# Optimization experiments

Hardware: AMD Instinct MI355X
Metric: run time of the kernel (lower is better)

## Reference

```python
import jax, jax.numpy as jnp
import numpy as np

N_HEAD = 8
D_IN = 128
D_KEY = 32
B = 65536
EPS = 1e-5
TEMP = float(D_KEY ** 0.5)


def _xavier(k, shape):
    fan_out, fan_in = shape
    limit = float(np.sqrt(6.0 / (fan_in + fan_out)))
    return jax.random.uniform(k, shape, jnp.float32, -limit, limit)


def setup_inputs() -> dict:
    key = jax.random.key(0)
    ks = jax.random.split(key, 6)
    return {
        "h_emb": jax.random.normal(ks[0], (B, D_IN), jnp.float32),
        "r_emb": jax.random.normal(ks[1], (B, D_IN), jnp.float32),
        "w_h": _xavier(ks[2], (N_HEAD * D_IN, D_IN)),
        "w_r": _xavier(ks[3], (N_HEAD * D_IN, D_IN)),
        "k_h": _xavier(ks[4], (D_KEY, D_IN)),
        "k_r": _xavier(ks[5], (D_KEY, D_IN)),
        "ln_gamma": jnp.ones((D_IN,), jnp.float32),
        "ln_beta": jnp.zeros((D_IN,), jnp.float32),
        "mode": 0,  # 0 == 'normal'
    }


def reference(h_emb, r_emb, w_h, w_r, k_h, k_r, ln_gamma, ln_beta, mode):
    # mode == 0 <=> 'normal': h_batch = h_emb.shape[0], r_batch = r_emb.shape[0]
    residual = h_emb                                     # [B, D]
    hb = h_emb.shape[0]
    rb = r_emb.shape[0]
    # linear projections to n_head copies: [1, B, H, D]
    h1 = (h_emb @ w_h.T).reshape(-1, hb, N_HEAD, D_IN)
    r1 = (r_emb @ w_r.T).reshape(-1, rb, N_HEAD, D_IN)
    # small key projections: [1, B, H, K]
    h1k = h1 @ k_h.T
    r1k = r1 @ k_r.T
    # tiny HxH attention per batch element: [1, B, H, H]
    xattn = jnp.einsum('gbhk,gbjk->gbhj', h1k / TEMP, r1k)
    g, b = xattn.shape[0], xattn.shape[1]
    xattn = jax.nn.softmax(xattn.reshape(g, b, N_HEAD * N_HEAD), axis=-1)
    xattn = xattn.reshape(g, b, N_HEAD, N_HEAD)
    h_x = xattn.sum(axis=-1)[..., None]                  # [1, B, H, 1]
    r_x = xattn.sum(axis=-2)[..., None]                  # [1, B, H, 1]
    # weighted combine + head-sum + residual: [1, B, D]
    t = (h1 * h_x + r1 * r_x).sum(axis=-2) + residual
    # LayerNorm (applied because norm_flag is False in the original)
    mu = t.mean(axis=-1, keepdims=True)
    var = ((t - mu) ** 2).mean(axis=-1, keepdims=True)
    return ln_gamma * (t - mu) / jnp.sqrt(var + EPS) + ln_beta
```

## Files before the change

kernel.cpp:

```cpp
#include <hip/hip_runtime.h>
#include <hip/hip_fp16.h>

#define TEMP_INV 0.17677669529663687f

typedef _Float16 f16x8 __attribute__((ext_vector_type(8)));
typedef float    f32x4 __attribute__((ext_vector_type(4)));

__device__ __forceinline__ ushort f2h(float x){
  __half h = __float2half(x);
  return __half_as_ushort(h);
}
__device__ __forceinline__ ushort4 f4h(float4 v){
  ushort4 o; o.x=f2h(v.x); o.y=f2h(v.y); o.z=f2h(v.z); o.w=f2h(v.w); return o;
}
__device__ __forceinline__ f16x8 cvt8(float4 a, float4 b){
  f16x8 r;
  r[0]=(_Float16)a.x; r[1]=(_Float16)a.y; r[2]=(_Float16)a.z; r[3]=(_Float16)a.w;
  r[4]=(_Float16)b.x; r[5]=(_Float16)b.y; r[6]=(_Float16)b.z; r[7]=(_Float16)b.w;
  return r;
}
__device__ __forceinline__ f16x8 vscale(f16x8 v, _Float16 s){
  f16x8 r;
  #pragma unroll
  for (int i=0;i<8;i++) r[i] = v[i]*s;
  return r;
}

__global__ void conv_w_kernel(const float* __restrict__ wh,
                              const float* __restrict__ wr,
                              ushort* __restrict__ w16h,
                              ushort* __restrict__ w16r){
  int t = blockIdx.x * 256 + threadIdx.x;
  int R  = t >> 5;
  int c4 = t & 31;
  int h  = R >> 7, np = R & 127;
  int kq = c4 >> 1, pos = (c4 & 1) * 4;
  int dst = ((h*16 + kq)*128 + np)*8 + pos;
  float4 a = ((const float4*)wh)[t];
  *(ushort4*)&w16h[dst] = f4h(a);
  float4 b = ((const float4*)wr)[t];
  *(ushort4*)&w16r[dst] = f4h(b);
}

__global__ void make_cw_kernel(const float* __restrict__ wh, const float* __restrict__ wr,
                               const float* __restrict__ kh, const float* __restrict__ kr,
                               ushort* __restrict__ cwh, ushort* __restrict__ cwr){
  int m  = blockIdx.x >> 5;
  int h  = (blockIdx.x >> 2) & 7;
  int iq = blockIdx.x & 3;
  const float* w = m ? wr : wh;
  const float* k = m ? kr : kh;
  ushort* cw = m ? cwr : cwh;

  extern __shared__ char smem[];
  float* w_s = (float*)smem;
  float* k_s = w_s + 128*32;
  int t = threadIdx.x;

  #pragma unroll
  for (int p=0;p<4;p++){
    int f = t + p*256;
    int d = f >> 3, c4 = f & 7;
    *(float4*)&w_s[d*32 + c4*4] =
        *(const float4*)&w[(size_t)(h*128 + d)*128 + iq*32 + c4*4];
  }
  #pragma unroll
  for (int p=0;p<4;p++){
    int f = t + p*256;
    ((float4*)k_s)[f] = ((const float4*)k)[f];
  }
  __syncthreads();

  int il  = t & 31;
  int kk0 = t >> 5;
  float acc[4] = {0.f,0.f,0.f,0.f};
  for (int d=0; d<128; d++){
    float wv = w_s[d*32 + il];
    #pragma unroll
    for (int j=0;j<4;j++) acc[j] += k_s[(kk0 + 8*j)*128 + d] * wv;
  }
  int i = iq*32 + il;
  #pragma unroll
  for (int j=0;j<4;j++){
    int n = h*32 + kk0 + 8*j;
    cw[(size_t)((i>>3)*256 + n)*8 + (i&7)] = f2h(acc[j]);
  }
}

__global__ __launch_bounds__(256,2) void xattn_fused(
    const float* __restrict__ h_emb, const float* __restrict__ r_emb,
    const ushort* __restrict__ w16h, const ushort* __restrict__ w16r,
    const ushort* __restrict__ cwh,  const ushort* __restrict__ cwr,
    const float* __restrict__ gamma, const float* __restrict__ beta,
    float* __restrict__ out)
{
  extern __shared__ char smem[];
  float* hk  = (float*)smem;
  float* rk  = hk + 32*292;
  float* hxs = rk + 32*292;
  float* rxs = hxs + 288;
  float* red = rxs + 288;

  const int t  = threadIdx.x;
  const int b0 = blockIdx.x * 32;
  const int l  = t & 63, w = t >> 6;
  const int g  = l >> 4, c = l & 15;

  f16x8 ah[2][4], ar[2][4];
  #pragma unroll
  for (int mt=0; mt<2; mt++){
    const float* ph = h_emb + ((size_t)(b0 + mt*16 + c))*128 + g*8;
    const float* pr = r_emb + ((size_t)(b0 + mt*16 + c))*128 + g*8;
    #pragma unroll
    for (int ks=0; ks<4; ks++){
      float4 lo  = *(const float4*)(ph + ks*32);
      float4 hi  = *(const float4*)(ph + ks*32 + 4);
      ah[mt][ks] = cvt8(lo, hi);
      float4 lo2 = *(const float4*)(pr + ks*32);
      float4 hi2 = *(const float4*)(pr + ks*32 + 4);
      ar[mt][ks] = cvt8(lo2, hi2);
    }
  }

  f32x4 aH[2][4] = {};
  f32x4 aR[2][4] = {};
  {
    const ushort* pH = cwh + ((size_t)g*256 + w*64 + c)*8;
    const ushort* pR = cwr + ((size_t)g*256 + w*64 + c)*8;
    #pragma unroll
    for (int ks=0; ks<4; ks++){
      #pragma unroll
      for (int nt=0; nt<4; nt++){
        f16x8 bh = *(const f16x8*)(pH + ((size_t)ks*1024 + nt*16)*8);
        f16x8 br = *(const f16x8*)(pR + ((size_t)ks*1024 + nt*16)*8);
        aH[0][nt] = __builtin_amdgcn_mfma_f32_16x16x32_f16(ah[0][ks], bh, aH[0][nt],0,0,0);
        aH[1][nt] = __builtin_amdgcn_mfma_f32_16x16x32_f16(ah[1][ks], bh, aH[1][nt],0,0,0);
        aR[0][nt] = __builtin_amdgcn_mfma_f32_16x16x32_f16(ar[0][ks], br, aR[0][nt],0,0,0);
        aR[1][nt] = __builtin_amdgcn_mfma_f32_16x16x32_f16(ar[1][ks], br, aR[1][nt],0,0,0);
      }
    }
  }

  #pragma unroll
  for (int mt=0; mt<2; mt++)
    #pragma unroll
    for (int nt=0; nt<4; nt++){
      int n  = w*64 + nt*16 + c;
      int hh = n >> 5, kk = n & 31;
      #pragma unroll
      for (int reg=0; reg<4; reg++){
        int e = mt*16 + g*4 + reg;
        hk[e*292 + hh*36 + kk] = aH[mt][nt][reg];
        rk[e*292 + hh*36 + kk] = aR[mt][nt][reg];
      }
    }
  __syncthreads();

  {
    int e = t >> 3, hr = t & 7;
    const float* hkr = &hk[e*292 + hr*36];
    float4 hv4[8];
    #pragma unroll
    for (int q=0;q<8;q++) hv4[q] = *(const float4*)&hkr[q*4];

    float lg[8];
    #pragma unroll
    for (int j=0;j<8;j++){
      const float* rkr = &rk[e*292 + j*36];
      float s = 0.f;
      #pragma unroll
      for (int q=0;q<8;q++){
        float4 rv = *(const float4*)&rkr[q*4];
        s += hv4[q].x*rv.x + hv4[q].y*rv.y + hv4[q].z*rv.z + hv4[q].w*rv.w;
      }
      lg[j] = s * TEMP_INV;
    }
    float mx = lg[0];
    #pragma unroll
    for (int j=1;j<8;j++) mx = fmaxf(mx, lg[j]);
    mx = fmaxf(mx, __shfl_xor(mx, 1));
    mx = fmaxf(mx, __shfl_xor(mx, 2));
    mx = fmaxf(mx, __shfl_xor(mx, 4));
    float p[8]; float srow = 0.f;
    #pragma unroll
    for (int j=0;j<8;j++){ p[j] = __expf(lg[j]-mx); srow += p[j]; }
    float S = srow;
    S += __shfl_xor(S, 1); S += __shfl_xor(S, 2); S += __shfl_xor(S, 4);
    float inv = 1.0f / S;
    hxs[e*9 + hr] = srow * inv;

    #pragma unroll
    for (int j=0;j<8;j++){
      p[j] += __shfl_xor(p[j], 1);
      p[j] += __shfl_xor(p[j], 2);
      p[j] += __shfl_xor(p[j], 4);
    }
    float cs = p[0];
    #pragma unroll
    for (int j=1;j<8;j++) cs = (hr==j) ? p[j] : cs;
    rxs[e*9 + hr] = cs * inv;
  }
  __syncthreads();

  const int col0 = w*32;
  f32x4 tacc[2][2] = {};
  {
    const ushort* bH = w16h + ((size_t)g*128 + col0 + c)*8;
    const ushort* bR = w16r + ((size_t)g*128 + col0 + c)*8;
    #pragma unroll
    for (int h=0; h<8; h++){
      _Float16 h0 = (_Float16)hxs[c*9 + h];
      _Float16 h1 = (_Float16)hxs[(16+c)*9 + h];
      _Float16 r0 = (_Float16)rxs[c*9 + h];
      _Float16 r1 = (_Float16)rxs[(16+c)*9 + h];
      #pragma unroll
      for (int ks=0; ks<4; ks++){
        size_t off = (size_t)(h*16 + ks*4)*128*8;
        f16x8 a0 = vscale(ah[0][ks], h0);
        f16x8 a1 = vscale(ah[1][ks], h1);
        f16x8 b0v = *(const f16x8*)(bH + off);
        f16x8 b1v = *(const f16x8*)(bH + off + 16*8);
        tacc[0][0] = __builtin_amdgcn_mfma_f32_16x16x32_f16(a0, b0v, tacc[0][0],0,0,0);
        tacc[1][0] = __builtin_amdgcn_mfma_f32_16x16x32_f16(a1, b0v, tacc[1][0],0,0,0);
        tacc[0][1] = __builtin_amdgcn_mfma_f32_16x16x32_f16(a0, b1v, tacc[0][1],0,0,0);
        tacc[1][1] = __builtin_amdgcn_mfma_f32_16x16x32_f16(a1, b1v, tacc[1][1],0,0,0);
        f16x8 c0 = vscale(ar[0][ks], r0);
        f16x8 c1 = vscale(ar[1][ks], r1);
        f16x8 d0v = *(const f16x8*)(bR + off);
        f16x8 d1v = *(const f16x8*)(bR + off + 16*8);
        tacc[0][0] = __builtin_amdgcn_mfma_f32_16x16x32_f16(c0, d0v, tacc[0][0],0,0,0);
        tacc[1][0] = __builtin_amdgcn_mfma_f32_16x16x32_f16(c1, d0v, tacc[1][0],0,0,0);
        tacc[0][1] = __builtin_amdgcn_mfma_f32_16x16x32_f16(c0, d1v, tacc[0][1],0,0,0);
        tacc[1][1] = __builtin_amdgcn_mfma_f32_16x16x32_f16(c1, d1v, tacc[1][1],0,0,0);
      }
    }
  }

  #pragma unroll
  for (int mt=0; mt<2; mt++)
    #pragma unroll
    for (int reg=0; reg<4; reg++){
      int row = mt*16 + g*4 + reg;
      const float* resid = h_emb + ((size_t)(b0+row))*128 + col0 + c;
      tacc[mt][0][reg] += resid[0];
      tacc[mt][1][reg] += resid[16];
    }

  #pragma unroll
  for (int mt=0; mt<2; mt++)
    #pragma unroll
    for (int reg=0; reg<4; reg++){
      float v0 = tacc[mt][0][reg], v1 = tacc[mt][1][reg];
      float a = v0 + v1, b2 = v0*v0 + v1*v1;
      #pragma unroll
      for (int m=1; m<16; m<<=1){
        a  += __shfl_xor(a,  m);
        b2 += __shfl_xor(b2, m);
      }
      if (c == 0){
        int row = mt*16 + g*4 + reg;
        red[row*8 + w*2]     = a;
        red[row*8 + w*2 + 1] = b2;
      }
    }
  __syncthreads();

  float gam0 = gamma[col0 + c],      bet0 = beta[col0 + c];
  float gam1 = gamma[col0 + 16 + c], bet1 = beta[col0 + 16 + c];
  #pragma unroll
  for (int mt=0; mt<2; mt++)
    #pragma unroll
    for (int reg=0; reg<4; reg++){
      int row = mt*16 + g*4 + reg;
      float S1 = red[row*8+0] + red[row*8+2] + red[row*8+4] + red[row*8+6];
      float S2 = red[row*8+1] + red[row*8+3] + red[row*8+5] + red[row*8+7];
      float mu  = S1 * 0.0078125f;
      float var = S2 * 0.0078125f - mu*mu;
      float rs  = rsqrtf(var + 1e-5f);
      float* po = out + ((size_t)(b0+row))*128 + col0 + c;
      po[0]  = gam0*((tacc[mt][0][reg]-mu)*rs) + bet0;
      po[16] = gam1*((tacc[mt][1][reg]-mu)*rs) + bet1;
    }
}

extern "C" void kernel_launch(void* const* d_in, const int* in_sizes, int n_in,
                              void* d_out, int out_size, void* d_ws, size_t ws_size,
                              hipStream_t stream){
  const float* h_emb = (const float*)d_in[0];
  const float* r_emb = (const float*)d_in[1];
  const float* w_h   = (const float*)d_in[2];
  const float* w_r   = (const float*)d_in[3];
  const float* k_h   = (const float*)d_in[4];
  const float* k_r   = (const float*)d_in[5];
  const float* gamma = (const float*)d_in[6];
  const float* beta  = (const float*)d_in[7];
  float* out = (float*)d_out;

  ushort* w16h = (ushort*)d_ws;
  ushort* w16r = w16h + 131072;
  ushort* cwh  = w16r + 131072;
  ushort* cwr  = cwh + 32768;

  conv_w_kernel<<<128, 256, 0, stream>>>(w_h, w_r, w16h, w16r);
  make_cw_kernel<<<64, 256, 32768, stream>>>(w_h, w_r, k_h, k_r, cwh, cwr);
  xattn_fused<<<2048, 256, 78080, stream>>>(h_emb, r_emb, w16h, w16r,
                                            cwh, cwr, gamma, beta, out);
}
```

Baseline: 209.6 us.

## Split fused kernel into attention and projection kernels with larger row tiles

Merges the two weight-prep kernels into one launch. Splits the fused kernel into an attention kernel (16 rows per block, writes per-row head weights to workspace) and a projection+LayerNorm kernel that handles 64 rows per block, so each loaded weight fragment feeds four row tiles. The goal is to cut repeated weight fetches and raise occupancy by shrinking shared memory. In exchange, h_emb and r_emb are read again in the second kernel and the head weights take an extra trip through global memory.

```diff
diff --git a/kernel.cpp b/kernel.cpp
--- a/kernel.cpp
+++ b/kernel.cpp
@@ -26,28 +26,27 @@
   return r;
 }
 
-__global__ void conv_w_kernel(const float* __restrict__ wh,
-                              const float* __restrict__ wr,
-                              ushort* __restrict__ w16h,
-                              ushort* __restrict__ w16r){
-  int t = blockIdx.x * 256 + threadIdx.x;
-  int R  = t >> 5;
-  int c4 = t & 31;
-  int h  = R >> 7, np = R & 127;
-  int kq = c4 >> 1, pos = (c4 & 1) * 4;
-  int dst = ((h*16 + kq)*128 + np)*8 + pos;
-  float4 a = ((const float4*)wh)[t];
-  *(ushort4*)&w16h[dst] = f4h(a);
-  float4 b = ((const float4*)wr)[t];
-  *(ushort4*)&w16r[dst] = f4h(b);
-}
-
-__global__ void make_cw_kernel(const float* __restrict__ wh, const float* __restrict__ wr,
-                               const float* __restrict__ kh, const float* __restrict__ kr,
-                               ushort* __restrict__ cwh, ushort* __restrict__ cwr){
-  int m  = blockIdx.x >> 5;
-  int h  = (blockIdx.x >> 2) & 7;
-  int iq = blockIdx.x & 3;
+__global__ void prep_kernel(const float* __restrict__ wh, const float* __restrict__ wr,
+                            const float* __restrict__ kh, const float* __restrict__ kr,
+                            ushort* __restrict__ w16h, ushort* __restrict__ w16r,
+                            ushort* __restrict__ cwh,  ushort* __restrict__ cwr){
+  if (blockIdx.x < 128){
+    int t = blockIdx.x * 256 + threadIdx.x;
+    int R  = t >> 5;
+    int c4 = t & 31;
+    int h  = R >> 7, np = R & 127;
+    int kq = c4 >> 1, pos = (c4 & 1) * 4;
+    int dst = ((h*16 + kq)*128 + np)*8 + pos;
+    float4 a = ((const float4*)wh)[t];
+    *(ushort4*)&w16h[dst] = f4h(a);
+    float4 b = ((const float4*)wr)[t];
+    *(ushort4*)&w16r[dst] = f4h(b);
+    return;
+  }
+  int bid = blockIdx.x - 128;
+  int m  = bid >> 5;
+  int h  = (bid >> 2) & 7;
+  int iq = bid & 3;
   const float* w = m ? wr : wh;
   const float* k = m ? kr : kh;
   ushort* cw = m ? cwr : cwh;
@@ -87,76 +86,65 @@
   }
 }
 
-__global__ __launch_bounds__(256,2) void xattn_fused(
+__global__ __launch_bounds__(256,4) void attn16_kernel(
     const float* __restrict__ h_emb, const float* __restrict__ r_emb,
-    const ushort* __restrict__ w16h, const ushort* __restrict__ w16r,
     const ushort* __restrict__ cwh,  const ushort* __restrict__ cwr,
-    const float* __restrict__ gamma, const float* __restrict__ beta,
-    float* __restrict__ out)
+    float* __restrict__ hx, float* __restrict__ rx)
 {
-  extern __shared__ char smem[];
-  float* hk  = (float*)smem;
-  float* rk  = hk + 32*292;
-  float* hxs = rk + 32*292;
-  float* rxs = hxs + 288;
-  float* red = rxs + 288;
+  __shared__ float hk[16*292];
+  __shared__ float rk[16*292];
 
   const int t  = threadIdx.x;
-  const int b0 = blockIdx.x * 32;
+  const int b0 = blockIdx.x * 16;
   const int l  = t & 63, w = t >> 6;
   const int g  = l >> 4, c = l & 15;
 
-  f16x8 ah[2][4], ar[2][4];
-  #pragma unroll
-  for (int mt=0; mt<2; mt++){
-    const float* ph = h_emb + ((size_t)(b0 + mt*16 + c))*128 + g*8;
-    const float* pr = r_emb + ((size_t)(b0 + mt*16 + c))*128 + g*8;
+  f16x8 ah[4], ar[4];
+  {
+    const float* ph = h_emb + ((size_t)(b0 + c))*128 + g*8;
+    const float* pr = r_emb + ((size_t)(b0 + c))*128 + g*8;
     #pragma unroll
     for (int ks=0; ks<4; ks++){
       float4 lo  = *(const float4*)(ph + ks*32);
       float4 hi  = *(const float4*)(ph + ks*32 + 4);
-      ah[mt][ks] = cvt8(lo, hi);
+      ah[ks] = cvt8(lo, hi);
       float4 lo2 = *(const float4*)(pr + ks*32);
       float4 hi2 = *(const float4*)(pr + ks*32 + 4);
-      ar[mt][ks] = cvt8(lo2, hi2);
-    }
-  }
-
-  f32x4 aH[2][4] = {};
-  f32x4 aR[2][4] = {};
+      ar[ks] = cvt8(lo2, hi2);
+    }
+  }
+
+  f32x4 aH[4] = {};
+  f32x4 aR[4] = {};
   {
-    const ushort* pH = cwh + ((size_t)g*256 + w*64 + c)*8;
-    const ushort* pR = cwr + ((size_t)g*256 + w*64 + c)*8;
+    const ushort* pH = cwh + ((size_t)(g*256 + w*64 + c))*8;
+    const ushort* pR = cwr + ((size_t)(g*256 + w*64 + c))*8;
     #pragma unroll
     for (int ks=0; ks<4; ks++){
       #pragma unroll
       for (int nt=0; nt<4; nt++){
-        f16x8 bh = *(const f16x8*)(pH + ((size_t)ks*1024 + nt*16)*8);
-        f16x8 br = *(const f16x8*)(pR + ((size_t)ks*1024 + nt*16)*8);
-        aH[0][nt] = __builtin_amdgcn_mfma_f32_16x16x32_f16(ah[0][ks], bh, aH[0][nt],0,0,0);
-        aH[1][nt] = __builtin_amdgcn_mfma_f32_16x16x32_f16(ah[1][ks], bh, aH[1][nt],0,0,0);
-        aR[0][nt] = __builtin_amdgcn_mfma_f32_16x16x32_f16(ar[0][ks], br, aR[0][nt],0,0,0);
-        aR[1][nt] = __builtin_amdgcn_mfma_f32_16x16x32_f16(ar[1][ks], br, aR[1][nt],0,0,0);
-      }
-    }
-  }
-
-  #pragma unroll
-  for (int mt=0; mt<2; mt++)
-    #pragma unroll
-    for (int nt=0; nt<4; nt++){
-      int n  = w*64 + nt*16 + c;
-      int hh = n >> 5, kk = n & 31;
-      #pragma unroll
-      for (int reg=0; reg<4; reg++){
-        int e = mt*16 + g*4 + reg;
-        hk[e*292 + hh*36 + kk] = aH[mt][nt][reg];
-        rk[e*292 + hh*36 + kk] = aR[mt][nt][reg];
-      }
-    }
+        f16x8 bh = *(const f16x8*)(pH + (size_t)(ks*1024 + nt*16)*8);
+        f16x8 br = *(const f16x8*)(pR + (size_t)(ks*1024 + nt*16)*8);
+        aH[nt] = __builtin_amdgcn_mfma_f32_16x16x32_f16(ah[ks], bh, aH[nt],0,0,0);
+        aR[nt] = __builtin_amdgcn_mfma_f32_16x16x32_f16(ar[ks], br, aR[nt],0,0,0);
+      }
+    }
+  }
+
+  #pragma unroll
+  for (int nt=0; nt<4; nt++){
+    int n  = w*64 + nt*16 + c;
+    int hh = n >> 5, kk = n & 31;
+    #pragma unroll
+    for (int reg=0; reg<4; reg++){
+      int e = g*4 + reg;
+      hk[e*292 + hh*36 + kk] = aH[nt][reg];
+      rk[e*292 + hh*36 + kk] = aR[nt][reg];
+    }
+  }
   __syncthreads();
 
-  {
+  if (t < 128){
     int e = t >> 3, hr = t & 7;
     const float* hkr = &hk[e*292 + hr*36];
     float4 hv4[8];
@@ -187,7 +175,7 @@
     float S = srow;
     S += __shfl_xor(S, 1); S += __shfl_xor(S, 2); S += __shfl_xor(S, 4);
     float inv = 1.0f / S;
-    hxs[e*9 + hr] = srow * inv;
+    hx[(size_t)(b0+e)*8 + hr] = srow * inv;
 
     #pragma unroll
     for (int j=0;j<8;j++){
@@ -198,59 +186,100 @@
     float cs = p[0];
     #pragma unroll
     for (int j=1;j<8;j++) cs = (hr==j) ? p[j] : cs;
-    rxs[e*9 + hr] = cs * inv;
+    rx[(size_t)(b0+e)*8 + hr] = cs * inv;
+  }
+}
+
+__global__ __launch_bounds__(256,3) void proj64_kernel(
+    const float* __restrict__ h_emb, const float* __restrict__ r_emb,
+    const ushort* __restrict__ w16h, const ushort* __restrict__ w16r,
+    const float* __restrict__ hx, const float* __restrict__ rx,
+    const float* __restrict__ gamma, const float* __restrict__ beta,
+    float* __restrict__ out)
+{
+  __shared__ float hxs[64*12];
+  __shared__ float rxs[64*12];
+  __shared__ float red[64*8];
+
+  const int t  = threadIdx.x;
+  const int b0 = blockIdx.x * 64;
+  const int l  = t & 63, w = t >> 6;
+  const int g  = l >> 4, c = l & 15;
+  const int col0 = w*32;
+
+  if (t < 128){
+    float4 v = ((const float4*)(hx + (size_t)b0*8))[t];
+    *(float4*)&hxs[(t>>1)*12 + (t&1)*4] = v;
+  } else {
+    int t2 = t - 128;
+    float4 v = ((const float4*)(rx + (size_t)b0*8))[t2];
+    *(float4*)&rxs[(t2>>1)*12 + (t2&1)*4] = v;
   }
   __syncthreads();
 
-  const int col0 = w*32;
-  f32x4 tacc[2][2] = {};
-  {
-    const ushort* bH = w16h + ((size_t)g*128 + col0 + c)*8;
-    const ushort* bR = w16r + ((size_t)g*128 + col0 + c)*8;
+  f32x4 tacc[4][2] = {};
+  f16x8 xa[4][4];
+
+  #pragma unroll
+  for (int pass=0; pass<2; pass++){
+    const float*  xsrc = pass ? r_emb : h_emb;
+    const ushort* wsrc = pass ? w16r  : w16h;
+    const float*  ssrc = pass ? rxs   : hxs;
+
+    #pragma unroll
+    for (int rf=0; rf<4; rf++){
+      const float* p = xsrc + ((size_t)(b0 + rf*16 + c))*128 + g*8;
+      #pragma unroll
+      for (int ks=0; ks<4; ks++){
+        float4 lo = *(const float4*)(p + ks*32);
+        float4 hi = *(const float4*)(p + ks*32 + 4);
+        xa[rf][ks] = cvt8(lo, hi);
+      }
+    }
+
+    const ushort* bW = wsrc + ((size_t)(g*128 + col0 + c))*8;
     #pragma unroll
     for (int h=0; h<8; h++){
-      _Float16 h0 = (_Float16)hxs[c*9 + h];
-      _Float16 h1 = (_Float16)hxs[(16+c)*9 + h];
-      _Float16 r0 = (_Float16)rxs[c*9 + h];
-      _Float16 r1 = (_Float16)rxs[(16+c)*9 + h];
+      _Float16 sc0 = (_Float16)ssrc[(     c)*12 + h];
+      _Float16 sc1 = (_Float16)ssrc[(16 + c)*12 + h];
+      _Float16 sc2 = (_Float16)ssrc[(32 + c)*12 + h];
+      _Float16 sc3 = (_Float16)ssrc[(48 + c)*12 + h];
       #pragma unroll
       for (int ks=0; ks<4; ks++){
-        size_t off = (size_t)(h*16 + ks*4)*128*8;
-        f16x8 a0 = vscale(ah[0][ks], h0);
-        f16x8 a1 = vscale(ah[1][ks], h1);
-        f16x8 b0v = *(const f16x8*)(bH + off);
-        f16x8 b1v = *(const f16x8*)(bH + off + 16*8);
+        size_t off = (size_t)((h*16 + ks*4)*128)*8;
+        f16x8 b0v = *(const f16x8*)(bW + off);
+        f16x8 b1v = *(const f16x8*)(bW + off + 16*8);
+        f16x8 a0 = vscale(xa[0][ks], sc0);
         tacc[0][0] = __builtin_amdgcn_mfma_f32_16x16x32_f16(a0, b0v, tacc[0][0],0,0,0);
+        tacc[0][1] = __builtin_amdgcn_mfma_f32_16x16x32_f16(a0, b1v, tacc[0][1],0,0,0);
+        f16x8 a1 = vscale(xa[1][ks], sc1);
         tacc[1][0] = __builtin_amdgcn_mfma_f32_16x16x32_f16(a1, b0v, tacc[1][0],0,0,0);
-        tacc[0][1] = __builtin_amdgcn_mfma_f32_16x16x32_f16(a0, b1v, tacc[0][1],0,0,0);
         tacc[1][1] = __builtin_amdgcn_mfma_f32_16x16x32_f16(a1, b1v, tacc[1][1],0,0,0);
-        f16x8 c0 = vscale(ar[0][ks], r0);
-        f16x8 c1 = vscale(ar[1][ks], r1);
-        f16x8 d0v = *(const f16x8*)(bR + off);
-        f16x8 d1v = *(const f16x8*)(bR + off + 16*8);
-        tacc[0][0] = __builtin_amdgcn_mfma_f32_16x16x32_f16(c0, d0v, tacc[0][0],0,0,0);
-        tacc[1][0] = __builtin_amdgcn_mfma_f32_16x16x32_f16(c1, d0v, tacc[1][0],0,0,0);
-        tacc[0][1] = __builtin_amdgcn_mfma_f32_16x16x32_f16(c0, d1v, tacc[0][1],0,0,0);
-        tacc[1][1] = __builtin_amdgcn_mfma_f32_16x16x32_f16(c1, d1v, tacc[1][1],0,0,0);
-      }
-    }
-  }
-
-  #pragma unroll
-  for (int mt=0; mt<2; mt++)
+        f16x8 a2 = vscale(xa[2][ks], sc2);
+        tacc[2][0] = __builtin_amdgcn_mfma_f32_16x16x32_f16(a2, b0v, tacc[2][0],0,0,0);
+        tacc[2][1] = __builtin_amdgcn_mfma_f32_16x16x32_f16(a2, b1v, tacc[2][1],0,0,0);
+        f16x8 a3 = vscale(xa[3][ks], sc3);
+        tacc[3][0] = __builtin_amdgcn_mfma_f32_16x16x32_f16(a3, b0v, tacc[3][0],0,0,0);
+        tacc[3][1] = __builtin_amdgcn_mfma_f32_16x16x32_f16(a3, b1v, tacc[3][1],0,0,0);
+      }
+    }
+  }
+
+  #pragma unroll
+  for (int rf=0; rf<4; rf++)
     #pragma unroll
     for (int reg=0; reg<4; reg++){
-      int row = mt*16 + g*4 + reg;
+      int row = rf*16 + g*4 + reg;
       const float* resid = h_emb + ((size_t)(b0+row))*128 + col0 + c;
-      tacc[mt][0][reg] += resid[0];
-      tacc[mt][1][reg] += resid[16];
-    }
-
-  #pragma unroll
-  for (int mt=0; mt<2; mt++)
+      tacc[rf][0][reg] += resid[0];
+      tacc[rf][1][reg] += resid[16];
+    }
+
+  #pragma unroll
+  for (int rf=0; rf<4; rf++)
     #pragma unroll
     for (int reg=0; reg<4; reg++){
-      float v0 = tacc[mt][0][reg], v1 = tacc[mt][1][reg];
+      float v0 = tacc[rf][0][reg], v1 = tacc[rf][1][reg];
       float a = v0 + v1, b2 = v0*v0 + v1*v1;
       #pragma unroll
       for (int m=1; m<16; m<<=1){
@@ -258,7 +287,7 @@
         b2 += __shfl_xor(b2, m);
       }
       if (c == 0){
-        int row = mt*16 + g*4 + reg;
+        int row = rf*16 + g*4 + reg;
         red[row*8 + w*2]     = a;
         red[row*8 + w*2 + 1] = b2;
       }
@@ -268,18 +297,18 @@
   float gam0 = gamma[col0 + c],      bet0 = beta[col0 + c];
   float gam1 = gamma[col0 + 16 + c], bet1 = beta[col0 + 16 + c];
   #pragma unroll
-  for (int mt=0; mt<2; mt++)
+  for (int rf=0; rf<4; rf++)
     #pragma unroll
     for (int reg=0; reg<4; reg++){
-      int row = mt*16 + g*4 + reg;
+      int row = rf*16 + g*4 + reg;
       float S1 = red[row*8+0] + red[row*8+2] + red[row*8+4] + red[row*8+6];
       float S2 = red[row*8+1] + red[row*8+3] + red[row*8+5] + red[row*8+7];
       float mu  = S1 * 0.0078125f;
       float var = S2 * 0.0078125f - mu*mu;
       float rs  = rsqrtf(var + 1e-5f);
       float* po = out + ((size_t)(b0+row))*128 + col0 + c;
-      po[0]  = gam0*((tacc[mt][0][reg]-mu)*rs) + bet0;
-      po[16] = gam1*((tacc[mt][1][reg]-mu)*rs) + bet1;
+      po[0]  = gam0*((tacc[rf][0][reg]-mu)*rs) + bet0;
+      po[16] = gam1*((tacc[rf][1][reg]-mu)*rs) + bet1;
     }
 }
 
@@ -300,9 +329,12 @@
   ushort* w16r = w16h + 131072;
   ushort* cwh  = w16r + 131072;
   ushort* cwr  = cwh + 32768;
-
-  conv_w_kernel<<<128, 256, 0, stream>>>(w_h, w_r, w16h, w16r);
-  make_cw_kernel<<<64, 256, 32768, stream>>>(w_h, w_r, k_h, k_r, cwh, cwr);
-  xattn_fused<<<2048, 256, 78080, stream>>>(h_emb, r_emb, w16h, w16r,
-                                            cwh, cwr, gamma, beta, out);
-}
+  float*  hxw  = (float*)(cwr + 32768);
+  float*  rxw  = hxw + 524288;
+
+  prep_kernel<<<192, 256, 32768, stream>>>(w_h, w_r, k_h, k_r,
+                                           w16h, w16r, cwh, cwr);
+  attn16_kernel<<<4096, 256, 0, stream>>>(h_emb, r_emb, cwh, cwr, hxw, rxw);
+  proj64_kernel<<<1024, 256, 0, stream>>>(h_emb, r_emb, w16h, w16r, hxw, rxw,
+                                          gamma, beta, out);
+}
```

Result: slower. 233.0 us (+11.2%).
